# Performance work log

Hardware: AMD Instinct MI355X
Metric: run time of the kernel (lower is better)

Reference implementation:

```python
import jax, jax.numpy as jnp
import numpy as np

H = 1024   # hidden_size
S = 32768  # seq_len


def setup_inputs() -> dict:
    key = jax.random.key(0)
    k1, k2, k3, k4 = jax.random.split(key, 4)
    scale = 1.0 / np.sqrt(H)
    return {
        "hidden": jax.random.normal(k1, (H,), dtype=jnp.float32),
        "encoder_outputs": jax.random.normal(k2, (S, H), dtype=jnp.float32),
        "W": jax.random.normal(k3, (H, H), dtype=jnp.float32) * scale,
        "b": jax.random.normal(k4, (H,), dtype=jnp.float32) * scale,
    }


def reference(hidden, encoder_outputs, W, b):
    # method == 'general': energy_i = W @ enc_i + b ; score_i = hidden . energy_i
    # Vectorized: scores = (enc @ W^T + b) @ hidden  -> [S]
    energies = jnp.einsum("sh,dh->sd", encoder_outputs, W) + b  # [S, H]
    scores = energies @ hidden                                   # [S]
    attn = jax.nn.softmax(scores)                                 # softmax over seq_len
    return attn[None, None, :]                                    # [1, 1, S]
```

## Files before the change

### kernel.cpp

```cpp
#include <hip/hip_runtime.h>
#include <math.h>

#define H 1024
#define S 32768
#define NPART 16
#define RPW 4
#define NB2 2048

#define WS_PART   0
#define WS_PM     16384
#define WS_PS     18432
#define WS_SCORES 20480

__global__ __launch_bounds__(256) void matvec_partial(const float* __restrict__ W,
                                                      const float* __restrict__ hidden,
                                                      float* __restrict__ ws) {
    float* part = ws + WS_PART;
    const int t  = threadIdx.x;
    const int l  = t & 63;
    const int dg = t >> 6;
    const int h  = blockIdx.x * 64 + l;
    const int d0 = blockIdx.y * 64 + dg * 16;

    float acc = 0.f;
#pragma unroll
    for (int i = 0; i < 16; ++i)
        acc += W[(size_t)(d0 + i) * H + h] * hidden[d0 + i];

    __shared__ float red[4][64];
    red[dg][l] = acc;
    __syncthreads();
    if (t < 64)
        part[blockIdx.y * H + blockIdx.x * 64 + l] =
            red[0][l] + red[1][l] + red[2][l] + red[3][l];
}

__device__ __forceinline__ float4 add4(float4 a, float4 b) {
    return make_float4(a.x + b.x, a.y + b.y, a.z + b.z, a.w + b.w);
}

__global__ __launch_bounds__(256, 4) void scores_partial(const float* __restrict__ enc,
                                                         float* __restrict__ ws) {
    float* scores = ws + WS_SCORES;
    float* pm     = ws + WS_PM;
    float* ps     = ws + WS_PS;
    const float* part = ws + WS_PART;

    const int tid  = threadIdx.x;
    const int lane = tid & 63;
    const int wv   = tid >> 6;
    const int blk  = blockIdx.x;
    const int gw   = blk * 4 + wv;
    const size_t row0 = (size_t)gw * RPW;

    __shared__ float vsh[H];
    {
        const float4* p4 = (const float4*)part;
        float4 t[NPART];
#pragma unroll
        for (int p = 0; p < NPART; ++p) t[p] = p4[p * (H / 4) + tid];
#pragma unroll
        for (int p = 0; p < 8; ++p) t[p] = add4(t[p], t[p + 8]);
#pragma unroll
        for (int p = 0; p < 4; ++p) t[p] = add4(t[p], t[p + 4]);
        ((float4*)vsh)[tid] = add4(add4(t[0], t[2]), add4(t[1], t[3]));
    }
    __syncthreads();

    const float4* e4 = (const float4*)(enc + row0 * H);
    float4 r[16];
#pragma unroll
    for (int it = 0; it < RPW; ++it)
#pragma unroll
        for (int k = 0; k < 4; ++k)
            r[it * 4 + k] = e4[it * 256 + k * 64 + lane];

    const float4* v4 = (const float4*)vsh;
    float4 vf[4];
#pragma unroll
    for (int k = 0; k < 4; ++k) vf[k] = v4[lane + 64 * k];

    float a[RPW];
#pragma unroll
    for (int it = 0; it < RPW; ++it) {
        const float4 e0 = r[it * 4 + 0], e1 = r[it * 4 + 1];
        const float4 e2 = r[it * 4 + 2], e3 = r[it * 4 + 3];
        float s0 = e0.x * vf[0].x + e0.y * vf[0].y + e0.z * vf[0].z + e0.w * vf[0].w;
        float s1 = e1.x * vf[1].x + e1.y * vf[1].y + e1.z * vf[1].z + e1.w * vf[1].w;
        float s2 = e2.x * vf[2].x + e2.y * vf[2].y + e2.z * vf[2].z + e2.w * vf[2].w;
        float s3 = e3.x * vf[3].x + e3.y * vf[3].y + e3.z * vf[3].z + e3.w * vf[3].w;
        a[it] = (s0 + s1) + (s2 + s3);
    }

#pragma unroll
    for (int it = 0; it < RPW; ++it) {
#pragma unroll
        for (int off = 32; off > 0; off >>= 1)
            a[it] += __shfl_xor(a[it], off, 64);
    }
    if (lane == 0)
        *(float4*)(scores + row0) = make_float4(a[0], a[1], a[2], a[3]);

    const float mw = fmaxf(fmaxf(a[0], a[1]), fmaxf(a[2], a[3]));
    float sw = __expf(a[0] - mw) + __expf(a[1] - mw) +
               __expf(a[2] - mw) + __expf(a[3] - mw);

    __shared__ float sm[4], ss[4];
    if (lane == 0) { sm[wv] = mw; ss[wv] = sw; }
    __syncthreads();
    if (tid == 0) {
        float m = sm[0], s = ss[0];
#pragma unroll
        for (int i = 1; i < 4; ++i) {
            const float nm = fmaxf(m, sm[i]);
            s = s * __expf(m - nm) + ss[i] * __expf(sm[i] - nm);
            m = nm;
        }
        pm[blk] = m; ps[blk] = s;
    }
}

__global__ __launch_bounds__(256) void finalize(const float* __restrict__ ws,
                                                float* __restrict__ out) {
    const float* scores = ws + WS_SCORES;
    const float* pm     = ws + WS_PM;
    const float* ps     = ws + WS_PS;

    const int tid  = threadIdx.x;
    const int lane = tid & 63;
    const int wv   = tid >> 6;

    float m = -INFINITY, s = 0.f;
#pragma unroll
    for (int i = 0; i < NB2 / 256; ++i) {
        const int idx = tid + i * 256;
        const float om = pm[idx], os = ps[idx];
        const float nm = fmaxf(m, om);
        s = s * __expf(m - nm) + os * __expf(om - nm);
        m = nm;
    }
#pragma unroll
    for (int off = 32; off > 0; off >>= 1) {
        const float om = __shfl_xor(m, off, 64);
        const float os = __shfl_xor(s, off, 64);
        const float nm = fmaxf(m, om);
        s = s * __expf(m - nm) + os * __expf(om - nm);
        m = nm;
    }
    __shared__ float sm[4], ss[4];
    if (lane == 0) { sm[wv] = m; ss[wv] = s; }
    __syncthreads();
    float M = sm[0], Ssum = ss[0];
#pragma unroll
    for (int i = 1; i < 4; ++i) {
        const float nm = fmaxf(M, sm[i]);
        Ssum = Ssum * __expf(M - nm) + ss[i] * __expf(sm[i] - nm);
        M = nm;
    }
    const float rs = 1.0f / Ssum;

    const int i = blockIdx.x * 256 + tid;
    out[i] = __expf(scores[i] - M) * rs;
}

extern "C" void kernel_launch(void* const* d_in, const int* in_sizes, int n_in,
                              void* d_out, int out_size, void* d_ws, size_t ws_size,
                              hipStream_t stream) {
    const float* hidden = (const float*)d_in[0];
    const float* enc    = (const float*)d_in[1];
    const float* W      = (const float*)d_in[2];
    float* out = (float*)d_out;
    float* ws  = (float*)d_ws;

    matvec_partial<<<dim3(16, 16), 256, 0, stream>>>(W, hidden, ws);
    scores_partial<<<NB2, 256, 0, stream>>>(enc, ws);
    finalize<<<S / 256, 256, 0, stream>>>(ws, out);
}
```

Before: 200.4 us.

## Stream encoder rows through double-buffered LDS tiles with global_load_lds

The scores kernel now gives each block 64 encoder rows instead of 16. It streams them in 8-row tiles into a double-buffered shared-memory buffer using direct global-to-LDS 16-byte loads, prefetching the next tile while the current one is reduced. The aim is to overlap memory traffic with compute and cut per-block setup, including the 16-way partial-vector reduction, by launching fewer blocks. In exchange it lowers occupancy to 2 blocks per CU and holds less data in flight per CU. Correctness also depends on the LDS DMA loads completing before the barrier-protected reads.

```diff
diff --git a/kernel.cpp b/kernel.cpp
--- a/kernel.cpp
+++ b/kernel.cpp
@@ -4,13 +4,15 @@
 #define H 1024
 #define S 32768
 #define NPART 16
-#define RPW 4
-#define NB2 2048
+#define NB2 512
+#define ROWS_PER_BLK 64
+#define TROWS 8
+#define NTILES 8
 
 #define WS_PART   0
 #define WS_PM     16384
-#define WS_PS     18432
-#define WS_SCORES 20480
+#define WS_PS     16896
+#define WS_SCORES 17408
 
 __global__ __launch_bounds__(256) void matvec_partial(const float* __restrict__ W,
                                                       const float* __restrict__ hidden,
@@ -39,7 +41,13 @@
     return make_float4(a.x + b.x, a.y + b.y, a.z + b.z, a.w + b.w);
 }
 
-__global__ __launch_bounds__(256, 4) void scores_partial(const float* __restrict__ enc,
+__device__ __forceinline__ void gload_lds16(const float* g, float* l) {
+    __builtin_amdgcn_global_load_lds(
+        (const __attribute__((address_space(1))) void*)g,
+        (__attribute__((address_space(3))) void*)l, 16, 0, 0);
+}
+
+__global__ __launch_bounds__(256, 2) void scores_partial(const float* __restrict__ enc,
                                                          float* __restrict__ ws) {
     float* scores = ws + WS_SCORES;
     float* pm     = ws + WS_PM;
@@ -50,10 +58,21 @@
     const int lane = tid & 63;
     const int wv   = tid >> 6;
     const int blk  = blockIdx.x;
-    const int gw   = blk * 4 + wv;
-    const size_t row0 = (size_t)gw * RPW;
-
+    const size_t row_base = (size_t)blk * ROWS_PER_BLK;
+
+    __shared__ float tile[2][TROWS * H];
     __shared__ float vsh[H];
+    __shared__ float sm[4], ss[4];
+
+    const float* enc_blk = enc + row_base * H;
+
+#pragma unroll
+    for (int i = 0; i < 8; ++i) {
+        const int c = wv * 8 + i;
+        gload_lds16(enc_blk + (size_t)(c >> 2) * H + (c & 3) * 256 + lane * 4,
+                    &tile[0][c * 256]);
+    }
+
     {
         const float4* p4 = (const float4*)part;
         float4 t[NPART];
@@ -67,45 +86,55 @@
     }
     __syncthreads();
 
-    const float4* e4 = (const float4*)(enc + row0 * H);
-    float4 r[16];
-#pragma unroll
-    for (int it = 0; it < RPW; ++it)
-#pragma unroll
-        for (int k = 0; k < 4; ++k)
-            r[it * 4 + k] = e4[it * 256 + k * 64 + lane];
-
-    const float4* v4 = (const float4*)vsh;
     float4 vf[4];
 #pragma unroll
-    for (int k = 0; k < 4; ++k) vf[k] = v4[lane + 64 * k];
-
-    float a[RPW];
-#pragma unroll
-    for (int it = 0; it < RPW; ++it) {
-        const float4 e0 = r[it * 4 + 0], e1 = r[it * 4 + 1];
-        const float4 e2 = r[it * 4 + 2], e3 = r[it * 4 + 3];
-        float s0 = e0.x * vf[0].x + e0.y * vf[0].y + e0.z * vf[0].z + e0.w * vf[0].w;
-        float s1 = e1.x * vf[1].x + e1.y * vf[1].y + e1.z * vf[1].z + e1.w * vf[1].w;
-        float s2 = e2.x * vf[2].x + e2.y * vf[2].y + e2.z * vf[2].z + e2.w * vf[2].w;
-        float s3 = e3.x * vf[3].x + e3.y * vf[3].y + e3.z * vf[3].z + e3.w * vf[3].w;
-        a[it] = (s0 + s1) + (s2 + s3);
-    }
-
-#pragma unroll
-    for (int it = 0; it < RPW; ++it) {
-#pragma unroll
-        for (int off = 32; off > 0; off >>= 1)
-            a[it] += __shfl_xor(a[it], off, 64);
-    }
-    if (lane == 0)
-        *(float4*)(scores + row0) = make_float4(a[0], a[1], a[2], a[3]);
-
-    const float mw = fmaxf(fmaxf(a[0], a[1]), fmaxf(a[2], a[3]));
-    float sw = __expf(a[0] - mw) + __expf(a[1] - mw) +
-               __expf(a[2] - mw) + __expf(a[3] - mw);
-
-    __shared__ float sm[4], ss[4];
+    for (int k = 0; k < 4; ++k) vf[k] = ((const float4*)vsh)[lane + 64 * k];
+
+    float sa[2 * NTILES];
+
+#pragma unroll
+    for (int t = 0; t < NTILES; ++t) {
+        if (t + 1 < NTILES) {
+            float* buf = tile[(t + 1) & 1];
+#pragma unroll
+            for (int i = 0; i < 8; ++i) {
+                const int c = wv * 8 + i;
+                gload_lds16(enc_blk + (size_t)((t + 1) * TROWS + (c >> 2)) * H +
+                                (c & 3) * 256 + lane * 4,
+                            &buf[c * 256]);
+            }
+        }
+
+        const float* tb = tile[t & 1];
+#pragma unroll
+        for (int j = 0; j < 2; ++j) {
+            const float4* r4 = (const float4*)(tb + (wv * 2 + j) * H);
+            const float4 e0 = r4[lane],       e1 = r4[lane + 64],
+                         e2 = r4[lane + 128], e3 = r4[lane + 192];
+            float s0 = e0.x * vf[0].x + e0.y * vf[0].y + e0.z * vf[0].z + e0.w * vf[0].w;
+            float s1 = e1.x * vf[1].x + e1.y * vf[1].y + e1.z * vf[1].z + e1.w * vf[1].w;
+            float s2 = e2.x * vf[2].x + e2.y * vf[2].y + e2.z * vf[2].z + e2.w * vf[2].w;
+            float s3 = e3.x * vf[3].x + e3.y * vf[3].y + e3.z * vf[3].z + e3.w * vf[3].w;
+            float a = (s0 + s1) + (s2 + s3);
+#pragma unroll
+            for (int off = 32; off > 0; off >>= 1)
+                a += __shfl_xor(a, off, 64);
+            sa[t * 2 + j] = a;
+        }
+        if (lane == 0)
+            *(float2*)(scores + row_base + t * TROWS + wv * 2) =
+                make_float2(sa[t * 2], sa[t * 2 + 1]);
+
+        __syncthreads();
+    }
+
+    float mw = sa[0];
+#pragma unroll
+    for (int i = 1; i < 2 * NTILES; ++i) mw = fmaxf(mw, sa[i]);
+    float sw = 0.f;
+#pragma unroll
+    for (int i = 0; i < 2 * NTILES; ++i) sw += __expf(sa[i] - mw);
+
     if (lane == 0) { sm[wv] = mw; ss[wv] = sw; }
     __syncthreads();
     if (tid == 0) {
```

Result: no change. 203.7 us (+1.7%).
